# Kernel tuning notes

Hardware: AMD Instinct MI355X
Metric: run time of the kernel (lower is better)

Reference implementation:

```python
import jax, jax.numpy as jnp
import numpy as np

EPS = 1e-06


def setup_inputs() -> dict:
    key = jax.random.key(0)
    k1, k2, k3, k4 = jax.random.split(key, 4)
    b, n, h, w = 16, 32, 256, 256
    pd = jax.random.uniform(k1, (b, h, w), dtype=jnp.float32)
    gt = jax.random.uniform(k2, (b, h, w), dtype=jnp.float32)
    pd_mask = jax.random.randint(k3, (b, n, h, w), 0, 2, dtype=jnp.int32)
    gt_mask = jax.random.randint(k4, (b, n, h, w), 0, 2, dtype=jnp.int32)
    return {"pd": pd, "gt": gt, "pd_mask": pd_mask, "gt_mask": gt_mask}


def reference(pd, gt, pd_mask, gt_mask):
    pdm = pd_mask.astype(bool)
    gtm = gt_mask.astype(bool)
    and_m = jnp.logical_and(pdm, gtm)            # pd & gt
    xor_m = jnp.logical_and(pdm, jnp.logical_not(gtm))  # (pd|gt) ^ gt == pd & ~gt
    f = pd.dtype
    # segmented masked sums over (h,w) for every (b, n) instance, fully vectorized
    inter = jnp.einsum('bhw,bnhw->bn', pd, and_m.astype(f))
    union = (jnp.einsum('bhw,bnhw->bn', gt, gtm.astype(f))
             + jnp.einsum('bhw,bnhw->bn', pd, xor_m.astype(f)))
    loss = inter / (union + EPS)
    return 1.0 - jnp.mean(loss)
```

## Files before the change

### kernel.cpp

```cpp
#include <hip/hip_runtime.h>

#define B 16
#define N 32
#define HW 65536
#define CHUNK 1024
#define CPB (HW / CHUNK)
#define NG 8
#define NGRP (N / NG)
#define NBLK (B * CPB * NGRP)
#define PAIRS (B * N)
#define EPS 1e-6f


__global__ __launch_bounds__(256, 4) void iou_partial_kernel(
    const float* __restrict__ pd, const float* __restrict__ gt,
    const int* __restrict__ pdm, const int* __restrict__ gtm,
    float2* __restrict__ ws)
{
    const int blk   = (blockIdx.x & 7) * (NBLK / 8) + (blockIdx.x >> 3);
    const int ng    = blk & (NGRP - 1);
    const int chunk = (blk >> 2) & (CPB - 1);
    const int b     = blk >> 8;
    const int t     = threadIdx.x;
    const int base  = chunk * CHUNK;

    const float4* __restrict__ pdp = (const float4*)(pd + (size_t)b * HW + base);
    const float4* __restrict__ gtp = (const float4*)(gt + (size_t)b * HW + base);
    const size_t mbase = (size_t)(b * N + ng * NG) * HW + base;
    const int4* __restrict__ pmp = (const int4*)(pdm + mbase);
    const int4* __restrict__ gmp = (const int4*)(gtm + mbase);

    const float4 p = pdp[t];
    const float4 g = gtp[t];

    float accI[NG], accU[NG];

    #pragma unroll
    for (int n = 0; n < NG; ++n) {
        const int o = n * (HW / 4);
        const int4 pm = pmp[o + t];
        const int4 gm = gmp[o + t];
        float I = 0.0f, U = 0.0f;
        I += (pm.x & gm.x) ? p.x : 0.0f;
        I += (pm.y & gm.y) ? p.y : 0.0f;
        I += (pm.z & gm.z) ? p.z : 0.0f;
        I += (pm.w & gm.w) ? p.w : 0.0f;
        U += gm.x ? g.x : (pm.x ? p.x : 0.0f);
        U += gm.y ? g.y : (pm.y ? p.y : 0.0f);
        U += gm.z ? g.z : (pm.z ? p.z : 0.0f);
        U += gm.w ? g.w : (pm.w ? p.w : 0.0f);
        accI[n] = I;
        accU[n] = U;
    }

    __shared__ float sI[4][NG], sU[4][NG];
    const int wave = t >> 6, lane = t & 63;
    #pragma unroll
    for (int n = 0; n < NG; ++n) {
        float I = accI[n], U = accU[n];
        #pragma unroll
        for (int o = 32; o > 0; o >>= 1) {
            I += __shfl_down(I, o, 64);
            U += __shfl_down(U, o, 64);
        }
        if (lane == 0) { sI[wave][n] = I; sU[wave][n] = U; }
    }
    __syncthreads();
    if (t < NG) {
        const float I = sI[0][t] + sI[1][t] + sI[2][t] + sI[3][t];
        const float U = sU[0][t] + sU[1][t] + sU[2][t] + sU[3][t];
        const int pair = b * N + ng * NG + t;
        ws[(size_t)pair * CPB + chunk] = make_float2(I, U);
    }
}

__global__ __launch_bounds__(512) void iou_final_kernel(
    const float2* __restrict__ ws, float* __restrict__ out)
{
    const int t = threadIdx.x;
    const float4* __restrict__ w4 = (const float4*)(ws + (size_t)t * CPB);
    float I = 0.0f, U = 0.0f;
    #pragma unroll
    for (int c = 0; c < CPB / 2; ++c) {
        const float4 v = w4[c];
        I += v.x + v.z;
        U += v.y + v.w;
    }
    float loss = I / (U + EPS);

    #pragma unroll
    for (int o = 32; o > 0; o >>= 1)
        loss += __shfl_down(loss, o, 64);

    __shared__ float s[8];
    const int wave = t >> 6, lane = t & 63;
    if (lane == 0) s[wave] = loss;
    __syncthreads();
    if (t == 0) {
        float sum = 0.0f;
        #pragma unroll
        for (int w = 0; w < 8; ++w) sum += s[w];
        out[0] = 1.0f - sum / (float)PAIRS;
    }
}

extern "C" void kernel_launch(void* const* d_in, const int* in_sizes, int n_in,
                              void* d_out, int out_size, void* d_ws, size_t ws_size,
                              hipStream_t stream) {
    const float* pd  = (const float*)d_in[0];
    const float* gt  = (const float*)d_in[1];
    const int*   pdm = (const int*)d_in[2];
    const int*   gtm = (const int*)d_in[3];
    float* out = (float*)d_out;
    float2* ws = (float2*)d_ws;

    iou_partial_kernel<<<NBLK, 256, 0, stream>>>(pd, gt, pdm, gtm, ws);
    iou_final_kernel<<<1, 512, 0, stream>>>(ws, out);
}
```

Measured before the change: 56.05 us.

## Process four chunks per block and restructure reductions and workspace layout

Each block now loops over four 1024-element chunks, which cuts the grid by four and accumulates per-thread sums across chunks before a single block reduction. The cross-wave reduction is rewritten to go through shared memory, with 32-lane shuffle groups handling one instance each. The workspace is transposed to chunk-group-major, so the final kernel does coalesced float4 reads across 16 groups with 256 threads. The intent is to cut block launch and reduction overhead and shrink the workspace, at the cost of fewer blocks and less memory-level parallelism, since the chunk loop is not unrolled.

```diff
diff --git a/kernel.cpp b/kernel.cpp
--- a/kernel.cpp
+++ b/kernel.cpp
@@ -4,10 +4,12 @@
 #define N 32
 #define HW 65536
 #define CHUNK 1024
+#define CI 4
 #define CPB (HW / CHUNK)
+#define CPG (CPB / CI)
 #define NG 8
 #define NGRP (N / NG)
-#define NBLK (B * CPB * NGRP)
+#define NBLK (B * CPG * NGRP)
 #define PAIRS (B * N)
 #define EPS 1e-6f
 
@@ -17,12 +19,12 @@
     const int* __restrict__ pdm, const int* __restrict__ gtm,
     float2* __restrict__ ws)
 {
-    const int blk   = (blockIdx.x & 7) * (NBLK / 8) + (blockIdx.x >> 3);
-    const int ng    = blk & (NGRP - 1);
-    const int chunk = (blk >> 2) & (CPB - 1);
-    const int b     = blk >> 8;
-    const int t     = threadIdx.x;
-    const int base  = chunk * CHUNK;
+    const int blk = (blockIdx.x & 7) * (NBLK / 8) + (blockIdx.x >> 3);
+    const int ng  = blk & (NGRP - 1);
+    const int cg  = (blk >> 2) & (CPG - 1);
+    const int b   = blk >> 6;
+    const int t   = threadIdx.x;
+    const int base = cg * (CHUNK * CI);
 
     const float4* __restrict__ pdp = (const float4*)(pd + (size_t)b * HW + base);
     const float4* __restrict__ gtp = (const float4*)(gt + (size_t)b * HW + base);
@@ -30,78 +32,80 @@
     const int4* __restrict__ pmp = (const int4*)(pdm + mbase);
     const int4* __restrict__ gmp = (const int4*)(gtm + mbase);
 
-    const float4 p = pdp[t];
-    const float4 g = gtp[t];
+    float accI[NG] = {0,0,0,0,0,0,0,0};
+    float accU[NG] = {0,0,0,0,0,0,0,0};
 
-    float accI[NG], accU[NG];
-
-    #pragma unroll
-    for (int n = 0; n < NG; ++n) {
-        const int o = n * (HW / 4);
-        const int4 pm = pmp[o + t];
-        const int4 gm = gmp[o + t];
-        float I = 0.0f, U = 0.0f;
-        I += (pm.x & gm.x) ? p.x : 0.0f;
-        I += (pm.y & gm.y) ? p.y : 0.0f;
-        I += (pm.z & gm.z) ? p.z : 0.0f;
-        I += (pm.w & gm.w) ? p.w : 0.0f;
-        U += gm.x ? g.x : (pm.x ? p.x : 0.0f);
-        U += gm.y ? g.y : (pm.y ? p.y : 0.0f);
-        U += gm.z ? g.z : (pm.z ? p.z : 0.0f);
-        U += gm.w ? g.w : (pm.w ? p.w : 0.0f);
-        accI[n] = I;
-        accU[n] = U;
+    #pragma unroll 1
+    for (int ci = 0; ci < CI; ++ci) {
+        const int idx = ci * (CHUNK / 4) + t;
+        const float4 p = pdp[idx];
+        const float4 g = gtp[idx];
+        #pragma unroll
+        for (int n = 0; n < NG; ++n) {
+            const int4 pm = pmp[n * (HW / 4) + idx];
+            const int4 gm = gmp[n * (HW / 4) + idx];
+            float I = 0.0f, U = 0.0f;
+            I += (pm.x & gm.x) ? p.x : 0.0f;
+            I += (pm.y & gm.y) ? p.y : 0.0f;
+            I += (pm.z & gm.z) ? p.z : 0.0f;
+            I += (pm.w & gm.w) ? p.w : 0.0f;
+            U += gm.x ? g.x : (pm.x ? p.x : 0.0f);
+            U += gm.y ? g.y : (pm.y ? p.y : 0.0f);
+            U += gm.z ? g.z : (pm.z ? p.z : 0.0f);
+            U += gm.w ? g.w : (pm.w ? p.w : 0.0f);
+            accI[n] += I;
+            accU[n] += U;
+        }
     }
 
-    __shared__ float sI[4][NG], sU[4][NG];
-    const int wave = t >> 6, lane = t & 63;
+    __shared__ float sI[NG][256], sU[NG][256];
     #pragma unroll
-    for (int n = 0; n < NG; ++n) {
-        float I = accI[n], U = accU[n];
-        #pragma unroll
-        for (int o = 32; o > 0; o >>= 1) {
-            I += __shfl_down(I, o, 64);
-            U += __shfl_down(U, o, 64);
-        }
-        if (lane == 0) { sI[wave][n] = I; sU[wave][n] = U; }
+    for (int n = 0; n < NG; ++n) { sI[n][t] = accI[n]; sU[n][t] = accU[n]; }
+    __syncthreads();
+
+    const int g8 = t >> 5;
+    const int l  = t & 31;
+    float I = 0.0f, U = 0.0f;
+    #pragma unroll
+    for (int k = 0; k < 8; ++k) {
+        I += sI[g8][l + 32 * k];
+        U += sU[g8][l + 32 * k];
     }
-    __syncthreads();
-    if (t < NG) {
-        const float I = sI[0][t] + sI[1][t] + sI[2][t] + sI[3][t];
-        const float U = sU[0][t] + sU[1][t] + sU[2][t] + sU[3][t];
-        const int pair = b * N + ng * NG + t;
-        ws[(size_t)pair * CPB + chunk] = make_float2(I, U);
+    #pragma unroll
+    for (int m = 16; m > 0; m >>= 1) {
+        I += __shfl_xor(I, m, 64);
+        U += __shfl_xor(U, m, 64);
+    }
+    if (l == 0) {
+        const int pair = b * N + ng * NG + g8;
+        ws[(size_t)cg * PAIRS + pair] = make_float2(I, U);
     }
 }
 
-__global__ __launch_bounds__(512) void iou_final_kernel(
+__global__ __launch_bounds__(256) void iou_final_kernel(
     const float2* __restrict__ ws, float* __restrict__ out)
 {
     const int t = threadIdx.x;
-    const float4* __restrict__ w4 = (const float4*)(ws + (size_t)t * CPB);
-    float I = 0.0f, U = 0.0f;
+    const float4* __restrict__ w4 = (const float4*)ws;
+    float I0 = 0.0f, U0 = 0.0f, I1 = 0.0f, U1 = 0.0f;
     #pragma unroll
-    for (int c = 0; c < CPB / 2; ++c) {
-        const float4 v = w4[c];
-        I += v.x + v.z;
-        U += v.y + v.w;
+    for (int cg = 0; cg < CPG; ++cg) {
+        const float4 v = w4[cg * (PAIRS / 2) + t];
+        I0 += v.x; U0 += v.y;
+        I1 += v.z; U1 += v.w;
     }
-    float loss = I / (U + EPS);
+    float loss = I0 / (U0 + EPS) + I1 / (U1 + EPS);
 
     #pragma unroll
     for (int o = 32; o > 0; o >>= 1)
         loss += __shfl_down(loss, o, 64);
 
-    __shared__ float s[8];
+    __shared__ float s[4];
     const int wave = t >> 6, lane = t & 63;
     if (lane == 0) s[wave] = loss;
     __syncthreads();
-    if (t == 0) {
-        float sum = 0.0f;
-        #pragma unroll
-        for (int w = 0; w < 8; ++w) sum += s[w];
-        out[0] = 1.0f - sum / (float)PAIRS;
-    }
+    if (t == 0)
+        out[0] = 1.0f - (s[0] + s[1] + s[2] + s[3]) / (float)PAIRS;
 }
 
 extern "C" void kernel_launch(void* const* d_in, const int* in_sizes, int n_in,
@@ -115,5 +119,5 @@
     float2* ws = (float2*)d_ws;
 
     iou_partial_kernel<<<NBLK, 256, 0, stream>>>(pd, gt, pdm, gtm, ws);
-    iou_final_kernel<<<1, 512, 0, stream>>>(ws, out);
+    iou_final_kernel<<<1, 256, 0, stream>>>(ws, out);
 }
```

After: 49.54 us. 11.6% less time.
